# Kernel optimization log

Hardware: AMD Instinct MI355X
Metric: run time of the kernel (lower is better)

The kernel has to match this reference:

```python
import jax, jax.numpy as jnp
import numpy as np

R = 16
LORA_ALPHA = 16
SCALING = LORA_ALPHA / R  # 1.0


def setup_inputs() -> dict:
    key = jax.random.key(0)
    kx, kr, ka = jax.random.split(key, 3)
    B, S, D, DO, E = 4, 2048, 4096, 4096, 8
    x = jax.random.normal(kx, (B, S, D), dtype=jnp.float32)
    # kaiming_uniform_(a=sqrt(5)) on Linear weight of fan_in=D -> U(-1/sqrt(D), 1/sqrt(D))
    bound_r = 1.0 / np.sqrt(D)
    route_w = jax.random.uniform(kr, (E, D), jnp.float32, -bound_r, bound_r)  # lora_route.weight
    bound_a = 1.0 / np.sqrt(D)
    A = jax.random.uniform(ka, (E, R, D), jnp.float32, -bound_a, bound_a)  # stacked lora_A{i}.weight [r, D]
    # lora_B weights are zero-initialized in the module; use small random for a nontrivial baseline
    kb = jax.random.fold_in(key, 7)
    Bw = jax.random.normal(kb, (E, DO, R), dtype=jnp.float32) * 0.02  # stacked lora_B{i}.weight [DO, r]
    return {"x": x, "route_w": route_w, "A": A, "Bw": Bw}


def reference(x, route_w, A, Bw):
    # router logits [B, S, E]
    logits = jnp.einsum("bsd,ed->bse", x, route_w)
    # top-1 hard routing: keep raw logit value at the argmax slot, zero elsewhere
    topk_v, topk_idx = jax.lax.top_k(logits, 1)  # [B,S,1]
    E = logits.shape[-1]
    route_weight = jax.nn.one_hot(topk_idx[..., 0], E, dtype=logits.dtype) * topk_v  # [B,S,E]
    # low-rank per-expert projections (dense over experts, as in the original loop)
    h = jnp.einsum("bsd,erd->bser", x, A)            # [B,S,E,r]
    wh = route_weight[..., None] * h                  # weight before the up-projection
    out = jnp.einsum("bser,eor->bso", wh, Bw) * SCALING  # [B,S,DO]
    return out
```

## Files before the change

kernel.cpp:

```cpp
#include <hip/hip_runtime.h>
#include <hip/hip_bf16.h>

#define DD   4096
#define NE   8
#define NR   16
#define NTOK 8192
#define NDO  4096
#define TAU  4e-4f
#define MAXFLAG 8000

typedef __attribute__((ext_vector_type(8))) __bf16 bf16x8;
typedef __attribute__((ext_vector_type(4))) float  f32x4;

__device__ __forceinline__ bf16x8 to_bf16x8(float4 a, float4 b) {
    bf16x8 r;
    r[0] = (__bf16)a.x; r[1] = (__bf16)a.y; r[2] = (__bf16)a.z; r[3] = (__bf16)a.w;
    r[4] = (__bf16)b.x; r[5] = (__bf16)b.y; r[6] = (__bf16)b.z; r[7] = (__bf16)b.w;
    return r;
}

__device__ __forceinline__ bf16x8 lo_bf16x8(float4 a, float4 b, bf16x8 h) {
    bf16x8 r;
    r[0] = (__bf16)(a.x - (float)h[0]); r[1] = (__bf16)(a.y - (float)h[1]);
    r[2] = (__bf16)(a.z - (float)h[2]); r[3] = (__bf16)(a.w - (float)h[3]);
    r[4] = (__bf16)(b.x - (float)h[4]); r[5] = (__bf16)(b.y - (float)h[5]);
    r[6] = (__bf16)(b.z - (float)h[6]); r[7] = (__bf16)(b.w - (float)h[7]);
    return r;
}

__global__ __launch_bounds__(1024) void k_route(const float* __restrict__ x,
                                                const float* __restrict__ rw,
                                                float* __restrict__ w_arr,
                                                int*   __restrict__ token_list,
                                                int*   __restrict__ count,
                                                int*   __restrict__ nflag,
                                                int*   __restrict__ flaglist) {
    const int t0   = blockIdx.x * 16;
    const int wv   = threadIdx.x >> 6;
    const int lane = threadIdx.x & 63;
    const int m    = lane & 15;
    const int half = lane >> 4;

    const float* xrow = x + (size_t)(t0 + m) * DD;
    const float* wrow = rw + (size_t)(m & 7) * DD;
    const bool   blo  = (m >> 3) != 0;

    f32x4 accH = {0.f,0.f,0.f,0.f}, accL = {0.f,0.f,0.f,0.f};
    const int kbase = wv * 256;
    #pragma unroll
    for (int ks = 0; ks < 8; ks++) {
        const int k0 = kbase + ks * 32 + half * 8;
        const float4 xa = *(const float4*)(xrow + k0);
        const float4 xb = *(const float4*)(xrow + k0 + 4);
        const float4 wa = *(const float4*)(wrow + k0);
        const float4 wb = *(const float4*)(wrow + k0 + 4);
        const bf16x8 xh = to_bf16x8(xa, xb);
        const bf16x8 xl = lo_bf16x8(xa, xb, xh);
        const bf16x8 wh = to_bf16x8(wa, wb);
        const bf16x8 bfrag = blo ? lo_bf16x8(wa, wb, wh) : wh;
        accH = __builtin_amdgcn_mfma_f32_16x16x32_bf16(xh, bfrag, accH, 0, 0, 0);
        accL = __builtin_amdgcn_mfma_f32_16x16x32_bf16(xl, bfrag, accL, 0, 0, 0);
    }

    __shared__ float Lred[16][16][17];
    #pragma unroll
    for (int r = 0; r < 4; r++)
        Lred[wv][half * 4 + r][m] = accH[r] + accL[r];
    __syncthreads();

    __shared__ float logit[16][NE];
    if (threadIdx.x < 128) {
        const int t = threadIdx.x >> 3, ee = threadIdx.x & 7;
        float s = 0.f;
        #pragma unroll
        for (int w = 0; w < 16; w++) s += Lred[w][t][ee] + Lred[w][t][ee + 8];
        logit[t][ee] = s;
    }
    __syncthreads();

    if (threadIdx.x < 16) {
        const int t = threadIdx.x;
        float best = -1e30f, second = -1e30f; int be = 0;
        #pragma unroll
        for (int e = 0; e < NE; e++) {
            const float s = logit[t][e];
            if (s > best) { second = best; best = s; be = e; }
            else if (s > second) { second = s; }
        }
        const int tok = t0 + t;
        w_arr[tok] = best;
        if (best - second < TAU) {
            const int p = atomicAdd(nflag, 1);
            if (p < MAXFLAG) flaglist[p] = tok;
        } else {
            const int p = atomicAdd(&count[be], 1);
            token_list[be * NTOK + p] = tok;
        }
    }
}

__global__ __launch_bounds__(256) void k_fix(const float* __restrict__ x,
                                             const float* __restrict__ rw,
                                             float* __restrict__ w_arr,
                                             int*   __restrict__ token_list,
                                             int*   __restrict__ count,
                                             const int* __restrict__ nflag,
                                             const int* __restrict__ flaglist) {
    const int wv   = threadIdx.x >> 6;
    const int lane = threadIdx.x & 63;
    int n = *nflag; if (n > MAXFLAG) n = MAXFLAG;

    for (int idx = blockIdx.x * 4 + wv; idx < n; idx += 128) {
        const int tok = flaglist[idx];
        const float* xp = x + (size_t)tok * DD;
        double acc[NE];
        #pragma unroll
        for (int e = 0; e < NE; e++) acc[e] = 0.0;
        for (int i = 0; i < 16; i++) {
            const int d4 = (i * 64 + lane) * 4;
            const float4 xv = *(const float4*)(xp + d4);
            const double x0 = xv.x, x1 = xv.y, x2 = xv.z, x3 = xv.w;
            #pragma unroll
            for (int e = 0; e < NE; e++) {
                const float4 wv4 = *(const float4*)(rw + (size_t)e * DD + d4);
                acc[e] = fma(x0, (double)wv4.x, acc[e]);
                acc[e] = fma(x1, (double)wv4.y, acc[e]);
                acc[e] = fma(x2, (double)wv4.z, acc[e]);
                acc[e] = fma(x3, (double)wv4.w, acc[e]);
            }
        }
        #pragma unroll
        for (int off = 32; off > 0; off >>= 1)
            #pragma unroll
            for (int e = 0; e < NE; e++)
                acc[e] += __shfl_xor(acc[e], off, 64);
        if (lane == 0) {
            double best = acc[0]; int be = 0;
            #pragma unroll
            for (int e = 1; e < NE; e++) if (acc[e] > best) { best = acc[e]; be = e; }
            w_arr[tok] = (float)best;
            const int pos = atomicAdd(&count[be], 1);
            token_list[be * NTOK + pos] = tok;
        }
    }
}

__global__ __launch_bounds__(1024) void k_h(const float* __restrict__ x,
                                            const float* __restrict__ Am,
                                            const float* __restrict__ w_arr,
                                            const int*   __restrict__ token_list,
                                            const int*   __restrict__ count,
                                            __hip_bfloat16* __restrict__ wh) {
    const int e    = blockIdx.x >> 7;
    const int g    = blockIdx.x & 127;
    const int cnt  = count[e];
    const int base = g * 32;
    if (base >= cnt) return;

    const int wv   = threadIdx.x >> 6;
    const int lane = threadIdx.x & 63;
    const int m    = lane & 15;
    const int half = lane >> 4;

    const int i0 = base + m,  i1 = base + 16 + m;
    const int tok0 = (i0 < cnt) ? token_list[e * NTOK + i0] : 0;
    const int tok1 = (i1 < cnt) ? token_list[e * NTOK + i1] : 0;
    const float* xr0  = x + (size_t)tok0 * DD;
    const float* xr1  = x + (size_t)tok1 * DD;
    const float* arow = Am + ((size_t)e * NR + m) * DD;

    f32x4 acc0 = {0.f,0.f,0.f,0.f}, acc1 = {0.f,0.f,0.f,0.f};
    const int kbase = wv * 256;
    #pragma unroll
    for (int kc = 0; kc < 8; kc++) {
        const int k0 = kbase + kc * 32 + half * 8;
        const bf16x8 bfrag = to_bf16x8(*(const float4*)(arow + k0),
                                       *(const float4*)(arow + k0 + 4));
        const bf16x8 a0 = to_bf16x8(*(const float4*)(xr0 + k0),
                                    *(const float4*)(xr0 + k0 + 4));
        const bf16x8 a1 = to_bf16x8(*(const float4*)(xr1 + k0),
                                    *(const float4*)(xr1 + k0 + 4));
        acc0 = __builtin_amdgcn_mfma_f32_16x16x32_bf16(a0, bfrag, acc0, 0, 0, 0);
        acc1 = __builtin_amdgcn_mfma_f32_16x16x32_bf16(a1, bfrag, acc1, 0, 0, 0);
    }

    __shared__ float lds[16][32][17];
    #pragma unroll
    for (int rr = 0; rr < 4; rr++) {
        lds[wv][half * 4 + rr][m]      = acc0[rr];
        lds[wv][16 + half * 4 + rr][m] = acc1[rr];
    }
    __syncthreads();

    if (threadIdx.x < 512) {
        const int t = threadIdx.x >> 4;
        const int r = threadIdx.x & 15;
        const int i2 = base + t;
        if (i2 < cnt) {
            float s = 0.f;
            #pragma unroll
            for (int w = 0; w < 16; w++) s += lds[w][t][r];
            const int tk = token_list[e * NTOK + i2];
            wh[(size_t)tk * NR + r] = (__hip_bfloat16)(s * w_arr[tk]);
        }
    }
}

__global__ __launch_bounds__(256) void k_out(const float* __restrict__ Bw,
                                             const __hip_bfloat16* __restrict__ wh,
                                             const int*   __restrict__ token_list,
                                             const int*   __restrict__ count,
                                             float* __restrict__ out) {
    const int bx    = blockIdx.x;
    const int chunk = bx & 3;
    const int slot  = (bx >> 2) & 511;
    const int e     = bx >> 11;
    const int cnt   = count[e];
    const int base  = slot * 16;
    if (base >= cnt) return;

    const int wv   = threadIdx.x >> 6;
    const int lane = threadIdx.x & 63;
    const int m    = lane & 15;
    const int half = lane >> 4;

    const int  idx   = base + m;
    const bool valid = idx < cnt;
    const int  tok   = valid ? token_list[e * NTOK + idx] : 0;

    bf16x8 a2;
    if (half < 2 && valid) {
        a2 = *(const bf16x8*)(wh + (size_t)tok * NR + half * 8);
    } else {
        #pragma unroll
        for (int j = 0; j < 8; j++) a2[j] = (__bf16)0.0f;
    }

    int trow[4]; bool vrow[4];
    #pragma unroll
    for (int r = 0; r < 4; r++) {
        const int ir = base + half * 4 + r;
        vrow[r] = ir < cnt;
        trow[r] = vrow[r] ? token_list[e * NTOK + ir] : 0;
    }

    const float* bwe = Bw + (size_t)e * NDO * NR;
    const int h2 = (half < 2) ? half : 0;
    const f32x4 zero4 = {0.f, 0.f, 0.f, 0.f};
    const int ob0 = chunk * 1024 + wv * 256;

    #pragma unroll 4
    for (int ot = 0; ot < 16; ot++) {
        const int obase = ob0 + ot * 16;
        const float* bp = bwe + (size_t)(obase + m) * NR + h2 * 8;
        const float4 p = *(const float4*)(bp);
        const float4 q = *(const float4*)(bp + 4);
        bf16x8 b2 = to_bf16x8(p, q);
        if (half >= 2) {
            #pragma unroll
            for (int j = 0; j < 8; j++) b2[j] = (__bf16)0.0f;
        }
        const f32x4 d = __builtin_amdgcn_mfma_f32_16x16x32_bf16(a2, b2, zero4, 0, 0, 0);
        #pragma unroll
        for (int r = 0; r < 4; r++) {
            if (vrow[r]) out[(size_t)trow[r] * NDO + obase + m] = d[r];
        }
    }
}

extern "C" void kernel_launch(void* const* d_in, const int* in_sizes, int n_in,
                              void* d_out, int out_size, void* d_ws, size_t ws_size,
                              hipStream_t stream) {
    const float* x  = (const float*)d_in[0];
    const float* rw = (const float*)d_in[1];
    const float* Am = (const float*)d_in[2];
    const float* Bw = (const float*)d_in[3];
    float* out = (float*)d_out;

    char* ws = (char*)d_ws;
    int*   count      = (int*)ws;
    int*   nflag      = (int*)(ws + 32);
    float* w_arr      = (float*)(ws + 512);
    int*   flaglist   = (int*)(ws + 33280);
    int*   token_list = (int*)(ws + 65536);
    __hip_bfloat16* wh = (__hip_bfloat16*)(ws + 65536 + NE * NTOK * 4);

    hipMemsetAsync(ws, 0, 64, stream);
    hipLaunchKernelGGL(k_route, dim3(512),   dim3(1024), 0, stream, x, rw, w_arr, token_list, count, nflag, flaglist);
    hipLaunchKernelGGL(k_fix,   dim3(32),    dim3(256),  0, stream, x, rw, w_arr, token_list, count, nflag, flaglist);
    hipLaunchKernelGGL(k_h,     dim3(1024),  dim3(1024), 0, stream, x, Am, w_arr, token_list, count, wh);
    hipLaunchKernelGGL(k_out,   dim3(16384), dim3(256),  0, stream, Bw, wh, token_list, count, out);
}
```

Measured before the change: 170.6 us.

## Rework routing and output kernels: bf16 Bw precast, token-ordered output, single-pass router

A new kernel precasts Bw to bf16, and a per-token expert id array is added. The output kernel now walks tokens in their natural order, 64 per block. For each token it runs all 8 experts' MFMAs, masking the A fragment by expert id, so stores are coalesced row writes rather than scattered gathers. The router stages x as bf16 in LDS and drops the low-part correction for x, keeping only the W split. The flag threshold is widened and the fix-up kernel gets more blocks to handle the extra near-tie tokens.

```diff
diff --git a/kernel.cpp b/kernel.cpp
--- a/kernel.cpp
+++ b/kernel.cpp
@@ -6,10 +6,11 @@
 #define NR   16
 #define NTOK 8192
 #define NDO  4096
-#define TAU  4e-4f
+#define TAU  0.01f
 #define MAXFLAG 8000
 
 typedef __attribute__((ext_vector_type(8))) __bf16 bf16x8;
+typedef __attribute__((ext_vector_type(4))) __bf16 bf16x4;
 typedef __attribute__((ext_vector_type(4))) float  f32x4;
 
 __device__ __forceinline__ bf16x8 to_bf16x8(float4 a, float4 b) {
@@ -28,9 +29,26 @@
     return r;
 }
 
+__device__ __forceinline__ bf16x8 zero_frag() {
+    bf16x8 z;
+    #pragma unroll
+    for (int j = 0; j < 8; j++) z[j] = (__bf16)0.0f;
+    return z;
+}
+
+__global__ __launch_bounds__(256) void k_bw(const float* __restrict__ Bw,
+                                            __bf16* __restrict__ Bwb) {
+    const int i = (blockIdx.x * 256 + threadIdx.x) * 4;
+    const float4 v = *(const float4*)(Bw + i);
+    bf16x4 p;
+    p[0] = (__bf16)v.x; p[1] = (__bf16)v.y; p[2] = (__bf16)v.z; p[3] = (__bf16)v.w;
+    *(bf16x4*)(Bwb + i) = p;
+}
+
 __global__ __launch_bounds__(1024) void k_route(const float* __restrict__ x,
                                                 const float* __restrict__ rw,
                                                 float* __restrict__ w_arr,
+                                                int*   __restrict__ eid,
                                                 int*   __restrict__ token_list,
                                                 int*   __restrict__ count,
                                                 int*   __restrict__ nflag,
@@ -41,40 +59,50 @@
     const int m    = lane & 15;
     const int half = lane >> 4;
 
-    const float* xrow = x + (size_t)(t0 + m) * DD;
-    const float* wrow = rw + (size_t)(m & 7) * DD;
-    const bool   blo  = (m >> 3) != 0;
-
-    f32x4 accH = {0.f,0.f,0.f,0.f}, accL = {0.f,0.f,0.f,0.f};
-    const int kbase = wv * 256;
-    #pragma unroll
-    for (int ks = 0; ks < 8; ks++) {
-        const int k0 = kbase + ks * 32 + half * 8;
-        const float4 xa = *(const float4*)(xrow + k0);
-        const float4 xb = *(const float4*)(xrow + k0 + 4);
-        const float4 wa = *(const float4*)(wrow + k0);
-        const float4 wb = *(const float4*)(wrow + k0 + 4);
-        const bf16x8 xh = to_bf16x8(xa, xb);
-        const bf16x8 xl = lo_bf16x8(xa, xb, xh);
-        const bf16x8 wh = to_bf16x8(wa, wb);
-        const bf16x8 bfrag = blo ? lo_bf16x8(wa, wb, wh) : wh;
-        accH = __builtin_amdgcn_mfma_f32_16x16x32_bf16(xh, bfrag, accH, 0, 0, 0);
-        accL = __builtin_amdgcn_mfma_f32_16x16x32_bf16(xl, bfrag, accL, 0, 0, 0);
-    }
-
-    __shared__ float Lred[16][16][17];
+    __shared__ __bf16 xt[16][1032];
+    __shared__ float  Lred[16][16][17];
+    __shared__ float  logitS[16][NE];
+
+    const float* xstage = x + (size_t)(t0 + wv) * DD;
+    const float* wrow   = rw + (size_t)(m & 7) * DD;
+    const bool   blo    = m >= 8;
+
+    f32x4 acc = {0.f, 0.f, 0.f, 0.f};
+
+    for (int c = 0; c < 4; c++) {
+        #pragma unroll
+        for (int p = 0; p < 2; p++) {
+            const int idx = p * 512 + lane * 8;
+            const float4 va = *(const float4*)(xstage + c * 1024 + idx);
+            const float4 vb = *(const float4*)(xstage + c * 1024 + idx + 4);
+            *(bf16x8*)&xt[wv][idx] = to_bf16x8(va, vb);
+        }
+        __syncthreads();
+        #pragma unroll
+        for (int ks = 0; ks < 2; ks++) {
+            const int kl = wv * 64 + ks * 32 + half * 8;
+            const bf16x8 a = *(const bf16x8*)&xt[m][kl];
+            const int kg = c * 1024 + kl;
+            const float4 wa = *(const float4*)(wrow + kg);
+            const float4 wb = *(const float4*)(wrow + kg + 4);
+            const bf16x8 bh = to_bf16x8(wa, wb);
+            const bf16x8 b  = blo ? lo_bf16x8(wa, wb, bh) : bh;
+            acc = __builtin_amdgcn_mfma_f32_16x16x32_bf16(a, b, acc, 0, 0, 0);
+        }
+        __syncthreads();
+    }
+
     #pragma unroll
     for (int r = 0; r < 4; r++)
-        Lred[wv][half * 4 + r][m] = accH[r] + accL[r];
+        Lred[wv][half * 4 + r][m] = acc[r];
     __syncthreads();
 
-    __shared__ float logit[16][NE];
     if (threadIdx.x < 128) {
         const int t = threadIdx.x >> 3, ee = threadIdx.x & 7;
         float s = 0.f;
         #pragma unroll
         for (int w = 0; w < 16; w++) s += Lred[w][t][ee] + Lred[w][t][ee + 8];
-        logit[t][ee] = s;
+        logitS[t][ee] = s;
     }
     __syncthreads();
 
@@ -83,7 +111,7 @@
         float best = -1e30f, second = -1e30f; int be = 0;
         #pragma unroll
         for (int e = 0; e < NE; e++) {
-            const float s = logit[t][e];
+            const float s = logitS[t][e];
             if (s > best) { second = best; best = s; be = e; }
             else if (s > second) { second = s; }
         }
@@ -93,6 +121,7 @@
             const int p = atomicAdd(nflag, 1);
             if (p < MAXFLAG) flaglist[p] = tok;
         } else {
+            eid[tok] = be;
             const int p = atomicAdd(&count[be], 1);
             token_list[be * NTOK + p] = tok;
         }
@@ -102,6 +131,7 @@
 __global__ __launch_bounds__(256) void k_fix(const float* __restrict__ x,
                                              const float* __restrict__ rw,
                                              float* __restrict__ w_arr,
+                                             int*   __restrict__ eid,
                                              int*   __restrict__ token_list,
                                              int*   __restrict__ count,
                                              const int* __restrict__ nflag,
@@ -110,7 +140,7 @@
     const int lane = threadIdx.x & 63;
     int n = *nflag; if (n > MAXFLAG) n = MAXFLAG;
 
-    for (int idx = blockIdx.x * 4 + wv; idx < n; idx += 128) {
+    for (int idx = blockIdx.x * 4 + wv; idx < n; idx += 512) {
         const int tok = flaglist[idx];
         const float* xp = x + (size_t)tok * DD;
         double acc[NE];
@@ -139,6 +169,7 @@
             #pragma unroll
             for (int e = 1; e < NE; e++) if (acc[e] > best) { best = acc[e]; be = e; }
             w_arr[tok] = (float)best;
+            eid[tok] = be;
             const int pos = atomicAdd(&count[be], 1);
             token_list[be * NTOK + pos] = tok;
         }
@@ -206,64 +237,51 @@
     }
 }
 
-__global__ __launch_bounds__(256) void k_out(const float* __restrict__ Bw,
+__global__ __launch_bounds__(512) void k_out(const __bf16* __restrict__ Bwb,
                                              const __hip_bfloat16* __restrict__ wh,
-                                             const int*   __restrict__ token_list,
-                                             const int*   __restrict__ count,
+                                             const int* __restrict__ eid,
                                              float* __restrict__ out) {
-    const int bx    = blockIdx.x;
-    const int chunk = bx & 3;
-    const int slot  = (bx >> 2) & 511;
-    const int e     = bx >> 11;
-    const int cnt   = count[e];
-    const int base  = slot * 16;
-    if (base >= cnt) return;
-
-    const int wv   = threadIdx.x >> 6;
-    const int lane = threadIdx.x & 63;
-    const int m    = lane & 15;
-    const int half = lane >> 4;
-
-    const int  idx   = base + m;
-    const bool valid = idx < cnt;
-    const int  tok   = valid ? token_list[e * NTOK + idx] : 0;
-
-    bf16x8 a2;
-    if (half < 2 && valid) {
-        a2 = *(const bf16x8*)(wh + (size_t)tok * NR + half * 8);
-    } else {
-        #pragma unroll
-        for (int j = 0; j < 8; j++) a2[j] = (__bf16)0.0f;
-    }
-
-    int trow[4]; bool vrow[4];
-    #pragma unroll
-    for (int r = 0; r < 4; r++) {
-        const int ir = base + half * 4 + r;
-        vrow[r] = ir < cnt;
-        trow[r] = vrow[r] ? token_list[e * NTOK + ir] : 0;
-    }
-
-    const float* bwe = Bw + (size_t)e * NDO * NR;
-    const int h2 = (half < 2) ? half : 0;
-    const f32x4 zero4 = {0.f, 0.f, 0.f, 0.f};
-    const int ob0 = chunk * 1024 + wv * 256;
-
-    #pragma unroll 4
-    for (int ot = 0; ot < 16; ot++) {
+    const int ochunk = blockIdx.x & 3;
+    const int t0     = (blockIdx.x >> 2) * 64;
+    const int wv     = threadIdx.x >> 6;
+    const int lane   = threadIdx.x & 63;
+    const int m      = lane & 15;
+    const int half   = lane >> 4;
+    const int h2     = (half < 2) ? half : 0;
+    const bf16x8 zf  = zero_frag();
+
+    bf16x8 a2[4]; int es[4];
+    #pragma unroll
+    for (int s = 0; s < 4; s++) {
+        const int tok = t0 + s * 16 + m;
+        es[s] = eid[tok];
+        a2[s] = (half < 2) ? *(const bf16x8*)((const __bf16*)wh + (size_t)tok * NR + half * 8)
+                           : zf;
+    }
+
+    const int ob0 = ochunk * 1024 + wv * 128;
+    #pragma unroll 2
+    for (int ot = 0; ot < 8; ot++) {
         const int obase = ob0 + ot * 16;
-        const float* bp = bwe + (size_t)(obase + m) * NR + h2 * 8;
-        const float4 p = *(const float4*)(bp);
-        const float4 q = *(const float4*)(bp + 4);
-        bf16x8 b2 = to_bf16x8(p, q);
-        if (half >= 2) {
-            #pragma unroll
-            for (int j = 0; j < 8; j++) b2[j] = (__bf16)0.0f;
-        }
-        const f32x4 d = __builtin_amdgcn_mfma_f32_16x16x32_bf16(a2, b2, zero4, 0, 0, 0);
+        f32x4 acc0 = {0.f,0.f,0.f,0.f}, acc1 = {0.f,0.f,0.f,0.f};
+        f32x4 acc2 = {0.f,0.f,0.f,0.f}, acc3 = {0.f,0.f,0.f,0.f};
+        #pragma unroll
+        for (int e = 0; e < NE; e++) {
+            const bf16x8 b2 = (half < 2)
+                ? *(const bf16x8*)(Bwb + ((size_t)e * NDO + obase + m) * NR + h2 * 8)
+                : zf;
+            acc0 = __builtin_amdgcn_mfma_f32_16x16x32_bf16(es[0] == e ? a2[0] : zf, b2, acc0, 0, 0, 0);
+            acc1 = __builtin_amdgcn_mfma_f32_16x16x32_bf16(es[1] == e ? a2[1] : zf, b2, acc1, 0, 0, 0);
+            acc2 = __builtin_amdgcn_mfma_f32_16x16x32_bf16(es[2] == e ? a2[2] : zf, b2, acc2, 0, 0, 0);
+            acc3 = __builtin_amdgcn_mfma_f32_16x16x32_bf16(es[3] == e ? a2[3] : zf, b2, acc3, 0, 0, 0);
+        }
+        const int rbase = t0 + half * 4;
         #pragma unroll
         for (int r = 0; r < 4; r++) {
-            if (vrow[r]) out[(size_t)trow[r] * NDO + obase + m] = d[r];
+            out[(size_t)(rbase +  0 + r) * NDO + obase + m] = acc0[r];
+            out[(size_t)(rbase + 16 + r) * NDO + obase + m] = acc1[r];
+            out[(size_t)(rbase + 32 + r) * NDO + obase + m] = acc2[r];
+            out[(size_t)(rbase + 48 + r) * NDO + obase + m] = acc3[r];
         }
     }
 }
@@ -283,11 +301,14 @@
     float* w_arr      = (float*)(ws + 512);
     int*   flaglist   = (int*)(ws + 33280);
     int*   token_list = (int*)(ws + 65536);
-    __hip_bfloat16* wh = (__hip_bfloat16*)(ws + 65536 + NE * NTOK * 4);
+    __hip_bfloat16* wh = (__hip_bfloat16*)(ws + 327680);
+    int*   eid        = (int*)(ws + 589824);
+    __bf16* Bwb       = (__bf16*)(ws + 622592);
 
     hipMemsetAsync(ws, 0, 64, stream);
-    hipLaunchKernelGGL(k_route, dim3(512),   dim3(1024), 0, stream, x, rw, w_arr, token_list, count, nflag, flaglist);
-    hipLaunchKernelGGL(k_fix,   dim3(32),    dim3(256),  0, stream, x, rw, w_arr, token_list, count, nflag, flaglist);
-    hipLaunchKernelGGL(k_h,     dim3(1024),  dim3(1024), 0, stream, x, Am, w_arr, token_list, count, wh);
-    hipLaunchKernelGGL(k_out,   dim3(16384), dim3(256),  0, stream, Bw, wh, token_list, count, out);
-}
+    hipLaunchKernelGGL(k_bw,    dim3(512),  dim3(256),  0, stream, Bw, Bwb);
+    hipLaunchKernelGGL(k_route, dim3(512),  dim3(1024), 0, stream, x, rw, w_arr, eid, token_list, count, nflag, flaglist);
+    hipLaunchKernelGGL(k_fix,   dim3(128),  dim3(256),  0, stream, x, rw, w_arr, eid, token_list, count, nflag, flaglist);
+    hipLaunchKernelGGL(k_h,     dim3(1024), dim3(1024), 0, stream, x, Am, w_arr, token_list, count, wh);
+    hipLaunchKernelGGL(k_out,   dim3(512),  dim3(512),  0, stream, Bwb, wh, eid, out);
+}
```

New measurement: 182.6 us. +7.0%, slower.
